# Kernel optimization log

Hardware: AMD Instinct MI355X
Metric: run time of the kernel (lower is better)

Reference implementation:

```python
import jax, jax.numpy as jnp
import numpy as np

POLY = jnp.array([-0.037, 0.481, -2.3, 4.917, -1.791], dtype=jnp.float32)


def adaptive_temperature_softmax(logits):
    # logits: [b, h, n, n]
    p = jax.nn.softmax(logits, axis=-1)
    entropy = jnp.sum(-p * jnp.log(p + 1e-9), axis=-1, keepdims=True)  # [b,h,n,1]
    poly = (POLY[0] * entropy**4 + POLY[1] * entropy**3
            + POLY[2] * entropy**2 + POLY[3] * entropy + POLY[4])
    beta = jnp.where(entropy > 0.5, jnp.maximum(poly, 1.0), 1.0)
    return jax.nn.softmax(logits * beta, axis=-1)


def setup_inputs() -> dict:
    key = jax.random.key(0)
    ks = jax.random.split(key, 5)
    b, n, dim = 2, 2048, 1024
    s = 0.02
    return {
        "x": jax.random.normal(ks[0], (b, n, dim), dtype=jnp.float32),
        "Wq": jax.random.normal(ks[1], (dim, dim), dtype=jnp.float32) * s,
        "Wk": jax.random.normal(ks[2], (dim, dim), dtype=jnp.float32) * s,
        "Wv": jax.random.normal(ks[3], (dim, dim), dtype=jnp.float32) * s,
        "Wo": jax.random.normal(ks[4], (dim, dim), dtype=jnp.float32) * s,
        "bo": jnp.zeros((dim,), dtype=jnp.float32),
    }


def reference(x, Wq, Wk, Wv, Wo, bo):
    b, n, dim = x.shape
    h = 16
    hd = dim // h

    def split_heads(t):  # [b,n,dim] -> [b,h,n,hd]
        return t.reshape(b, n, h, hd).transpose(0, 2, 1, 3)

    # torch Linear: y = x @ W.T
    q = split_heads(x @ Wq.T)
    k = split_heads(x @ Wk.T)
    v = split_heads(x @ Wv.T)

    sim = jnp.einsum('bhid,bhjd->bhij', q, k) / jnp.sqrt(jnp.float32(hd))
    causal = jnp.triu(jnp.ones((n, n), dtype=bool), 1)
    neg = -jnp.finfo(sim.dtype).max
    sim = jnp.where(causal, neg, sim)

    attn = adaptive_temperature_softmax(sim)
    out = jnp.einsum('bhij,bhjd->bhid', attn, v)
    out = out.transpose(0, 2, 1, 3).reshape(b, n, dim)
    return out @ Wo.T + bo
```

## Files before the change

kernel.cpp:

```cpp
#include <hip/hip_runtime.h>
#include <hip/hip_bf16.h>

typedef __attribute__((ext_vector_type(8))) short bf16x8;
typedef __attribute__((ext_vector_type(4))) short short4v;
typedef __attribute__((ext_vector_type(4))) float f32x4;
typedef unsigned int u32;

__device__ __forceinline__ short f2bf(float f) {
    union { float f; u32 i; } c; c.f = f;
    u32 r = c.i + 0x7FFFu + ((c.i >> 16) & 1u);
    return (short)(r >> 16);
}
__device__ __forceinline__ u32 pack2bf(float lo, float hi) {
    return ((u32)(unsigned short)f2bf(hi) << 16) | (u32)(unsigned short)f2bf(lo);
}
__device__ __forceinline__ f32x4 mfma16(bf16x8 a, bf16x8 b, f32x4 c) {
    return __builtin_amdgcn_mfma_f32_16x16x32_bf16(a, b, c, 0, 0, 0);
}
__device__ __forceinline__ f32x4 mfma16k16(short4v a, short4v b, f32x4 c) {
#if __has_builtin(__builtin_amdgcn_mfma_f32_16x16x16bf16_1k)
    return __builtin_amdgcn_mfma_f32_16x16x16bf16_1k(a, b, c, 0, 0, 0);
#else
    f32x4 d = c;
    asm volatile("v_mfma_f32_16x16x16_bf16 %0, %1, %2, %0"
                 : "+v"(d) : "v"(a), "v"(b));
    return d;
#endif
}
__device__ __forceinline__ void load_lds16(const void* g, void* l) {
    __builtin_amdgcn_global_load_lds(
        (const __attribute__((address_space(1))) u32*)g,
        (__attribute__((address_space(3))) u32*)l, 16, 0, 0);
}

__global__ __launch_bounds__(256) void cvt_all_kernel(
    const float* __restrict__ x, const float* __restrict__ wq,
    const float* __restrict__ wk, const float* __restrict__ wv,
    const float* __restrict__ wo, short* __restrict__ ws) {
    const int XV = (4096 * 1024) / 4;
    const int WV = (1024 * 1024) / 4;
    int i = blockIdx.x * 256 + threadIdx.x;
    const float4* src; short4v* dst; int off;
    if (i < XV)            { src = (const float4*)x;  dst = (short4v*)(ws);           off = i; }
    else if (i < XV + WV)  { src = (const float4*)wq; dst = (short4v*)(ws + 4194304); off = i - XV; }
    else if (i < XV + 2*WV){ src = (const float4*)wk; dst = (short4v*)(ws + 5242880); off = i - XV - WV; }
    else if (i < XV + 3*WV){ src = (const float4*)wv; dst = (short4v*)(ws + 6291456); off = i - XV - 2*WV; }
    else                   { src = (const float4*)wo; dst = (short4v*)(ws + 7340032); off = i - XV - 3*WV; }
    float4 v = src[off];
    short4v o;
    o.x = f2bf(v.x); o.y = f2bf(v.y); o.z = f2bf(v.z); o.w = f2bf(v.w);
    dst[off] = o;
}

__device__ __forceinline__ void gemm_mainloop(
    const short* __restrict__ A, const short* __restrict__ Bm,
    short* lds, int mbase, int nbase, int wave, int lane, f32x4 acc[4][4]) {
    const int K = 1024;
    const int lr = lane & 15, lg = lane >> 4;
    const int wm = wave >> 1, wn = wave & 1;
    for (int k0 = 0; k0 < K; k0 += 64) {
        __syncthreads();
        #pragma unroll
        for (int issue = 0; issue < 4; ++issue) {
            int f = issue * 4 + wave;
            int mt = f >> 1, kc = f & 1;
            load_lds16(A  + (size_t)(mbase + mt*16 + lr)*K + (k0 + kc*32 + lg*8), lds + f*512);
            load_lds16(Bm + (size_t)(nbase + mt*16 + lr)*K + (k0 + kc*32 + lg*8), lds + 8192 + f*512);
        }
        __syncthreads();
        #pragma unroll
        for (int kc = 0; kc < 2; ++kc) {
            bf16x8 af[4], bfv[4];
            #pragma unroll
            for (int mi = 0; mi < 4; ++mi)
                af[mi] = *(const bf16x8*)(lds + ((wm*4 + mi)*2 + kc)*512 + lane*8);
            #pragma unroll
            for (int ni = 0; ni < 4; ++ni)
                bfv[ni] = *(const bf16x8*)(lds + 8192 + ((wn*4 + ni)*2 + kc)*512 + lane*8);
            #pragma unroll
            for (int mi = 0; mi < 4; ++mi)
                #pragma unroll
                for (int ni = 0; ni < 4; ++ni)
                    acc[mi][ni] = mfma16(af[mi], bfv[ni], acc[mi][ni]);
        }
    }
}

__global__ __launch_bounds__(256) void gemm_qkv_kernel(
    const short* __restrict__ xb, const short* __restrict__ wqb,
    const short* __restrict__ wkb, const short* __restrict__ wvb,
    short* __restrict__ Qh, short* __restrict__ Kh, short* __restrict__ Vf) {
    __shared__ short lds[16896];
    const int wave = threadIdx.x >> 6, lane = threadIdx.x & 63;
    const int lr = lane & 15, lg = lane >> 4;
    const int sel = blockIdx.x >> 3;
    const int nbase = (blockIdx.x & 7) * 128;
    const int mbase = blockIdx.y * 128;
    const short* Bm = (sel == 0) ? wqb : (sel == 1) ? wkb : wvb;

    f32x4 acc[4][4];
    #pragma unroll
    for (int i = 0; i < 4; ++i)
        #pragma unroll
        for (int j = 0; j < 4; ++j) acc[i][j] = f32x4{0.f, 0.f, 0.f, 0.f};

    gemm_mainloop(xb, Bm, lds, mbase, nbase, wave, lane, acc);

    const int wm = wave >> 1, wn = wave & 1;
    if (sel == 2) {
        #pragma unroll
        for (int mi = 0; mi < 4; ++mi) {
            int m0 = mbase + wm*64 + mi*16 + lg*4;
            #pragma unroll
            for (int ni = 0; ni < 4; ++ni) {
                int nc = nbase + wn*64 + ni*16 + lr;
                int h = nc >> 6, d = nc & 63;
                f32x4 v = acc[mi][ni];
                int bi = m0 >> 11, np = m0 & 2047;
                int c = np >> 6, s = (np >> 4) & 3, lg2 = (np >> 2) & 3;
                int dc = d >> 4, lr2 = d & 15;
                size_t off = ((size_t)(bi*16 + h)*32 + c)*4096
                           + (size_t)((s*4 + dc)*64 + lg2*16 + lr2)*4;
                short4v o;
                o.x = f2bf(v.x); o.y = f2bf(v.y); o.z = f2bf(v.z); o.w = f2bf(v.w);
                *(short4v*)&Vf[off] = o;
            }
        }
    } else {
        short* dstb = (sel == 0) ? Qh : Kh;
        const float sc = (sel == 0) ? 0.125f : 1.0f;
        __syncthreads();
        #pragma unroll
        for (int mi = 0; mi < 4; ++mi) {
            int row0 = wm*64 + mi*16 + lg*4;
            #pragma unroll
            for (int ni = 0; ni < 4; ++ni) {
                int col = wn*64 + ni*16 + lr;
                f32x4 v = acc[mi][ni];
                #pragma unroll
                for (int r = 0; r < 4; ++r)
                    lds[(row0 + r)*132 + col] = f2bf(v[r] * sc);
            }
        }
        __syncthreads();
        const int h0 = nbase >> 6;
        const int tid = threadIdx.x;
        #pragma unroll
        for (int it = 0; it < 8; ++it) {
            int L = it*256 + tid;
            int np_l = L >> 4;
            int t16 = L & 15;
            int P = t16 >> 3;
            int c8 = (t16 & 7) * 8;
            bf16x8 val = *(const bf16x8*)&lds[np_l*132 + P*64 + c8];
            int m = mbase + np_l; int bi = m >> 11, np = m & 2047;
            *(bf16x8*)&dstb[((size_t)(bi*16 + h0 + P)*2048 + np)*64 + c8] = val;
        }
    }
}

__global__ __launch_bounds__(256) void gemm_out_kernel(
    const short* __restrict__ AO, const short* __restrict__ wob,
    const float* __restrict__ bias, float* __restrict__ out) {
    __shared__ short lds[12288];
    const int K = 1024;
    const int wave = threadIdx.x >> 6, lane = threadIdx.x & 63;
    const int lr = lane & 15, lg = lane >> 4;
    const int nbase = blockIdx.x * 128;
    const int mbase = blockIdx.y * 64;
    const int wm = wave >> 1, wn = wave & 1;

    f32x4 acc[2][4];
    #pragma unroll
    for (int i = 0; i < 2; ++i)
        #pragma unroll
        for (int j = 0; j < 4; ++j) acc[i][j] = f32x4{0.f, 0.f, 0.f, 0.f};

    for (int k0 = 0; k0 < K; k0 += 64) {
        __syncthreads();
        #pragma unroll
        for (int l = 0; l < 6; ++l) {
            int f = l*4 + wave;
            if (f < 8) {
                int mt = f >> 1, kc = f & 1;
                load_lds16(AO + (size_t)(mbase + mt*16 + lr)*K + (k0 + kc*32 + lg*8),
                           lds + f*512);
            } else {
                int fb = f - 8, nt = fb >> 1, kc = fb & 1;
                load_lds16(wob + (size_t)(nbase + nt*16 + lr)*K + (k0 + kc*32 + lg*8),
                           lds + 4096 + fb*512);
            }
        }
        __syncthreads();
        #pragma unroll
        for (int kc = 0; kc < 2; ++kc) {
            bf16x8 af[2], bfv[4];
            #pragma unroll
            for (int mi = 0; mi < 2; ++mi)
                af[mi] = *(const bf16x8*)(lds + ((wm*2 + mi)*2 + kc)*512 + lane*8);
            #pragma unroll
            for (int ni = 0; ni < 4; ++ni)
                bfv[ni] = *(const bf16x8*)(lds + 4096 + ((wn*4 + ni)*2 + kc)*512 + lane*8);
            #pragma unroll
            for (int mi = 0; mi < 2; ++mi)
                #pragma unroll
                for (int ni = 0; ni < 4; ++ni)
                    acc[mi][ni] = mfma16(af[mi], bfv[ni], acc[mi][ni]);
        }
    }

    #pragma unroll
    for (int mi = 0; mi < 2; ++mi) {
        int m0 = mbase + wm*32 + mi*16 + lg*4;
        #pragma unroll
        for (int ni = 0; ni < 4; ++ni) {
            int nc = nbase + wn*64 + ni*16 + lr;
            float bj = bias[nc];
            f32x4 v = acc[mi][ni];
            #pragma unroll
            for (int r = 0; r < 4; ++r)
                out[(size_t)(m0 + r)*1024 + nc] = v[r] + bj;
        }
    }
}

__global__ __launch_bounds__(256, 4) void attn_kernel(
    const short* __restrict__ Qh, const short* __restrict__ Kh,
    const short* __restrict__ Vf, short* __restrict__ AO) {
    __shared__ short lds[16384];
    const int lane = threadIdx.x & 63;
    const int wave = threadIdx.x >> 6;
    const int lr = lane & 15, lg = lane >> 4;
    const int bid  = blockIdx.x;
    const int xcd  = bid & 7;
    const int rest = bid >> 3;
    const int u    = 31 - (rest >> 2);
    const int bh   = ((rest & 3) << 3) | xcd;
    const int b = bh >> 4, h = bh & 15;
    const int qbase = u*64 + wave*16;
    const int qa = qbase + lr;
    const short* Q  = Qh + (size_t)bh * (2048 * 64);
    const short* Kg = Kh + (size_t)bh * (2048 * 64);
    const short* Vg = Vf + (size_t)bh * (32 * 4096);

    bf16x8 qf0 = *(const bf16x8*)&Q[(size_t)qa*64 + lg*8];
    bf16x8 qf1 = *(const bf16x8*)&Q[(size_t)qa*64 + 32 + lg*8];

    const int fc0 = wave * 2;

    auto stageK = [&](int buf, int c) {
        #pragma unroll
        for (int i = 0; i < 2; ++i) {
            int fc = fc0 + i, s = fc >> 1, ch = fc & 1;
            load_lds16(Kg + ((size_t)(c*64 + s*16 + lr)*64 + ch*32 + lg*8),
                       &lds[buf*4096 + fc*512]);
        }
    };
    auto stageV = [&](int buf, int c) {
        #pragma unroll
        for (int i = 0; i < 2; ++i) {
            int fi = fc0 + i;
            load_lds16(Vg + (size_t)c*4096 + fi*512 + lane*8,
                       &lds[8192 + buf*4096 + fi*512]);
        }
    };

    float sm = 0.f, tm = 0.f;
    stageK(0, 0);
    #pragma unroll 1
    for (int c = 0; c <= u; ++c) {
        __syncthreads();
        if (c < u) stageK((c + 1) & 1, c + 1);
        const int base = (c & 1) * 4096;
        #pragma unroll
        for (int s = 0; s < 4; ++s) {
            int k0 = c*64 + s*16;
            if (k0 <= qbase) {
                bf16x8 kf0 = *(const bf16x8*)&lds[base + (s*2    )*512 + lane*8];
                bf16x8 kf1 = *(const bf16x8*)&lds[base + (s*2 + 1)*512 + lane*8];
                f32x4 d = {0.f,0.f,0.f,0.f};
                d = mfma16(kf0, qf0, d); d = mfma16(kf1, qf1, d);
                if (k0 < qbase) {
                    #pragma unroll
                    for (int r = 0; r < 4; ++r) {
                        float e = __expf(d[r]); sm += e; tm += e * d[r];
                    }
                } else {
                    int kb = k0 + lg*4;
                    #pragma unroll
                    for (int r = 0; r < 4; ++r) {
                        float l = (kb + r <= qa) ? d[r] : -1e30f;
                        float e = __expf(l); sm += e; tm += e * l;
                    }
                }
            }
        }
    }
    sm += __shfl_xor(sm, 16); tm += __shfl_xor(tm, 16);
    sm += __shfl_xor(sm, 32); tm += __shfl_xor(tm, 32);
    float H = __logf(sm) - tm / sm;
    float beta = 1.f;
    if (H > 0.5f)
        beta = fmaxf((((-0.037f*H + 0.481f)*H - 2.3f)*H + 4.917f)*H - 1.791f, 1.f);

    f32x4 o0 = {0.f,0.f,0.f,0.f}, o1 = {0.f,0.f,0.f,0.f};
    f32x4 o2 = {0.f,0.f,0.f,0.f}, o3 = {0.f,0.f,0.f,0.f};
    float s2 = 0.f;
    __syncthreads();
    stageK(0, 0); stageV(0, 0);
    #pragma unroll 1
    for (int c = 0; c <= u; ++c) {
        __syncthreads();
        if (c < u) { stageK((c + 1) & 1, c + 1); stageV((c + 1) & 1, c + 1); }
        const int kb_ = (c & 1) * 4096;
        const int vb_ = 8192 + (c & 1) * 4096;
        #pragma unroll
        for (int s = 0; s < 4; ++s) {
            int k0 = c*64 + s*16;
            if (k0 <= qbase) {
                bf16x8 kf0 = *(const bf16x8*)&lds[kb_ + (s*2    )*512 + lane*8];
                bf16x8 kf1 = *(const bf16x8*)&lds[kb_ + (s*2 + 1)*512 + lane*8];
                f32x4 d = {0.f,0.f,0.f,0.f};
                d = mfma16(kf0, qf0, d); d = mfma16(kf1, qf1, d);
                float pv[4];
                if (k0 < qbase) {
                    #pragma unroll
                    for (int r = 0; r < 4; ++r) { pv[r] = __expf(beta * d[r]); s2 += pv[r]; }
                } else {
                    int kb = k0 + lg*4;
                    #pragma unroll
                    for (int r = 0; r < 4; ++r) {
                        pv[r] = (kb + r <= qa) ? __expf(beta * d[r]) : 0.f; s2 += pv[r];
                    }
                }
                union { short4v s4; u32 uu[2]; } pb;
                pb.uu[0] = pack2bf(pv[0], pv[1]);
                pb.uu[1] = pack2bf(pv[2], pv[3]);
                short4v vf0 = *(const short4v*)&lds[vb_ + ((s*4 + 0)*64 + lane)*4];
                short4v vf1 = *(const short4v*)&lds[vb_ + ((s*4 + 1)*64 + lane)*4];
                short4v vf2 = *(const short4v*)&lds[vb_ + ((s*4 + 2)*64 + lane)*4];
                short4v vf3 = *(const short4v*)&lds[vb_ + ((s*4 + 3)*64 + lane)*4];
                o0 = mfma16k16(vf0, pb.s4, o0);
                o1 = mfma16k16(vf1, pb.s4, o1);
                o2 = mfma16k16(vf2, pb.s4, o2);
                o3 = mfma16k16(vf3, pb.s4, o3);
            }
        }
    }
    s2 += __shfl_xor(s2, 16); s2 += __shfl_xor(s2, 32);
    float inv = 1.f / s2;

    size_t row = ((size_t)(b*2048 + qa))*1024 + h*64;
    f32x4 oo[4] = {o0, o1, o2, o3};
    #pragma unroll
    for (int dc = 0; dc < 4; ++dc) {
        short4v wv;
        #pragma unroll
        for (int r = 0; r < 4; ++r) wv[r] = f2bf(oo[dc][r] * inv);
        *(short4v*)&AO[row + dc*16 + lg*4] = wv;
    }
}

extern "C" void kernel_launch(void* const* d_in, const int* in_sizes, int n_in,
                              void* d_out, int out_size, void* d_ws, size_t ws_size,
                              hipStream_t stream) {
    const float* x  = (const float*)d_in[0];
    const float* Wq = (const float*)d_in[1];
    const float* Wk = (const float*)d_in[2];
    const float* Wv = (const float*)d_in[3];
    const float* Wo = (const float*)d_in[4];
    const float* bo = (const float*)d_in[5];
    float* out = (float*)d_out;
    short* ws = (short*)d_ws;

    short* xb  = ws;
    short* wqb = ws + 4194304;
    short* wkb = ws + 5242880;
    short* wvb = ws + 6291456;
    short* wob = ws + 7340032;
    short* Qh  = ws + 8388608;
    short* Kh  = ws + 12582912;
    short* Vf  = ws + 16777216;
    short* AO  = ws + 20971520;

    cvt_all_kernel<<<8192, 256, 0, stream>>>(x, Wq, Wk, Wv, Wo, ws);
    gemm_qkv_kernel<<<dim3(24, 32), 256, 0, stream>>>(xb, wqb, wkb, wvb, Qh, Kh, Vf);
    attn_kernel<<<1024, 256, 0, stream>>>(Qh, Kh, Vf, AO);
    gemm_out_kernel<<<dim3(8, 64), 256, 0, stream>>>(AO, wob, bo, out);
}
```

Before: 158.2 us.

## Fold log2e into Q scale for exp2 softmax and halve QKV GEMM M-tile

Q is pre-scaled by log2(e) in the QKV GEMM epilogue so the attention kernel can use raw v_exp_f32 (exp2) in place of __expf, and the entropy is recomputed in base 2 then converted back with ln2. The QKV projection GEMM tile drops from 128x128 to 64x128, doubling the grid to 1536 blocks to raise occupancy and CU coverage on the 4096x1024x3072 problem. The exp change removes a multiply per exponential in the two softmax passes. The smaller tile lowers data reuse per block and adds more global loads.

```diff
diff --git a/kernel.cpp b/kernel.cpp
--- a/kernel.cpp
+++ b/kernel.cpp
@@ -25,6 +25,13 @@
     asm volatile("v_mfma_f32_16x16x16_bf16 %0, %1, %2, %0"
                  : "+v"(d) : "v"(a), "v"(b));
     return d;
+#endif
+}
+__device__ __forceinline__ float fexp2(float x) {
+#if __has_builtin(__builtin_amdgcn_exp2f)
+    return __builtin_amdgcn_exp2f(x);
+#else
+    float r; asm("v_exp_f32 %0, %1" : "=v"(r) : "v"(x)); return r;
 #endif
 }
 __device__ __forceinline__ void load_lds16(const void* g, void* l) {
@@ -52,65 +59,63 @@
     dst[off] = o;
 }
 
-__device__ __forceinline__ void gemm_mainloop(
-    const short* __restrict__ A, const short* __restrict__ Bm,
-    short* lds, int mbase, int nbase, int wave, int lane, f32x4 acc[4][4]) {
-    const int K = 1024;
-    const int lr = lane & 15, lg = lane >> 4;
-    const int wm = wave >> 1, wn = wave & 1;
-    for (int k0 = 0; k0 < K; k0 += 64) {
-        __syncthreads();
-        #pragma unroll
-        for (int issue = 0; issue < 4; ++issue) {
-            int f = issue * 4 + wave;
-            int mt = f >> 1, kc = f & 1;
-            load_lds16(A  + (size_t)(mbase + mt*16 + lr)*K + (k0 + kc*32 + lg*8), lds + f*512);
-            load_lds16(Bm + (size_t)(nbase + mt*16 + lr)*K + (k0 + kc*32 + lg*8), lds + 8192 + f*512);
-        }
-        __syncthreads();
-        #pragma unroll
-        for (int kc = 0; kc < 2; ++kc) {
-            bf16x8 af[4], bfv[4];
-            #pragma unroll
-            for (int mi = 0; mi < 4; ++mi)
-                af[mi] = *(const bf16x8*)(lds + ((wm*4 + mi)*2 + kc)*512 + lane*8);
-            #pragma unroll
-            for (int ni = 0; ni < 4; ++ni)
-                bfv[ni] = *(const bf16x8*)(lds + 8192 + ((wn*4 + ni)*2 + kc)*512 + lane*8);
-            #pragma unroll
-            for (int mi = 0; mi < 4; ++mi)
-                #pragma unroll
-                for (int ni = 0; ni < 4; ++ni)
-                    acc[mi][ni] = mfma16(af[mi], bfv[ni], acc[mi][ni]);
-        }
-    }
-}
-
 __global__ __launch_bounds__(256) void gemm_qkv_kernel(
     const short* __restrict__ xb, const short* __restrict__ wqb,
     const short* __restrict__ wkb, const short* __restrict__ wvb,
     short* __restrict__ Qh, short* __restrict__ Kh, short* __restrict__ Vf) {
-    __shared__ short lds[16896];
+    __shared__ short lds[12288];
+    const int K = 1024;
     const int wave = threadIdx.x >> 6, lane = threadIdx.x & 63;
     const int lr = lane & 15, lg = lane >> 4;
     const int sel = blockIdx.x >> 3;
     const int nbase = (blockIdx.x & 7) * 128;
-    const int mbase = blockIdx.y * 128;
+    const int mbase = blockIdx.y * 64;
     const short* Bm = (sel == 0) ? wqb : (sel == 1) ? wkb : wvb;
-
-    f32x4 acc[4][4];
+    const int wm = wave >> 1, wn = wave & 1;
+
+    f32x4 acc[2][4];
     #pragma unroll
-    for (int i = 0; i < 4; ++i)
+    for (int i = 0; i < 2; ++i)
         #pragma unroll
         for (int j = 0; j < 4; ++j) acc[i][j] = f32x4{0.f, 0.f, 0.f, 0.f};
 
-    gemm_mainloop(xb, Bm, lds, mbase, nbase, wave, lane, acc);
-
-    const int wm = wave >> 1, wn = wave & 1;
+    for (int k0 = 0; k0 < K; k0 += 64) {
+        __syncthreads();
+        #pragma unroll
+        for (int l = 0; l < 6; ++l) {
+            int f = l*4 + wave;
+            if (f < 8) {
+                int mt = f >> 1, kc = f & 1;
+                load_lds16(xb + (size_t)(mbase + mt*16 + lr)*K + (k0 + kc*32 + lg*8),
+                           lds + f*512);
+            } else {
+                int fb = f - 8, nt = fb >> 1, kc = fb & 1;
+                load_lds16(Bm + (size_t)(nbase + nt*16 + lr)*K + (k0 + kc*32 + lg*8),
+                           lds + 4096 + fb*512);
+            }
+        }
+        __syncthreads();
+        #pragma unroll
+        for (int kc = 0; kc < 2; ++kc) {
+            bf16x8 af[2], bfv[4];
+            #pragma unroll
+            for (int mi = 0; mi < 2; ++mi)
+                af[mi] = *(const bf16x8*)(lds + ((wm*2 + mi)*2 + kc)*512 + lane*8);
+            #pragma unroll
+            for (int ni = 0; ni < 4; ++ni)
+                bfv[ni] = *(const bf16x8*)(lds + 4096 + ((wn*4 + ni)*2 + kc)*512 + lane*8);
+            #pragma unroll
+            for (int mi = 0; mi < 2; ++mi)
+                #pragma unroll
+                for (int ni = 0; ni < 4; ++ni)
+                    acc[mi][ni] = mfma16(af[mi], bfv[ni], acc[mi][ni]);
+        }
+    }
+
     if (sel == 2) {
         #pragma unroll
-        for (int mi = 0; mi < 4; ++mi) {
-            int m0 = mbase + wm*64 + mi*16 + lg*4;
+        for (int mi = 0; mi < 2; ++mi) {
+            int m0 = mbase + wm*32 + mi*16 + lg*4;
             #pragma unroll
             for (int ni = 0; ni < 4; ++ni) {
                 int nc = nbase + wn*64 + ni*16 + lr;
@@ -128,11 +133,11 @@
         }
     } else {
         short* dstb = (sel == 0) ? Qh : Kh;
-        const float sc = (sel == 0) ? 0.125f : 1.0f;
-        __syncthreads();
-        #pragma unroll
-        for (int mi = 0; mi < 4; ++mi) {
-            int row0 = wm*64 + mi*16 + lg*4;
+        const float sc = (sel == 0) ? 0.125f * 1.44269504f : 1.0f;
+        __syncthreads();
+        #pragma unroll
+        for (int mi = 0; mi < 2; ++mi) {
+            int row0 = wm*32 + mi*16 + lg*4;
             #pragma unroll
             for (int ni = 0; ni < 4; ++ni) {
                 int col = wn*64 + ni*16 + lr;
@@ -146,10 +151,10 @@
         const int h0 = nbase >> 6;
         const int tid = threadIdx.x;
         #pragma unroll
-        for (int it = 0; it < 8; ++it) {
-            int L = it*256 + tid;
-            int np_l = L >> 4;
-            int t16 = L & 15;
+        for (int it = 0; it < 4; ++it) {
+            int g = it*256 + tid;
+            int np_l = g >> 4;
+            int t16 = g & 15;
             int P = t16 >> 3;
             int c8 = (t16 & 7) * 8;
             bf16x8 val = *(const bf16x8*)&lds[np_l*132 + P*64 + c8];
@@ -265,7 +270,7 @@
         }
     };
 
-    float sm = 0.f, tm = 0.f;
+    float sm = 0.f, t2m = 0.f;
     stageK(0, 0);
     #pragma unroll 1
     for (int c = 0; c <= u; ++c) {
@@ -283,22 +288,23 @@
                 if (k0 < qbase) {
                     #pragma unroll
                     for (int r = 0; r < 4; ++r) {
-                        float e = __expf(d[r]); sm += e; tm += e * d[r];
+                        float e = fexp2(d[r]); sm += e; t2m += e * d[r];
                     }
                 } else {
                     int kb = k0 + lg*4;
                     #pragma unroll
                     for (int r = 0; r < 4; ++r) {
-                        float l = (kb + r <= qa) ? d[r] : -1e30f;
-                        float e = __expf(l); sm += e; tm += e * l;
+                        float dd = (kb + r <= qa) ? d[r] : -1e30f;
+                        float e = fexp2(dd); sm += e; t2m += e * dd;
                     }
                 }
             }
         }
     }
-    sm += __shfl_xor(sm, 16); tm += __shfl_xor(tm, 16);
-    sm += __shfl_xor(sm, 32); tm += __shfl_xor(tm, 32);
-    float H = __logf(sm) - tm / sm;
+    sm += __shfl_xor(sm, 16); t2m += __shfl_xor(t2m, 16);
+    sm += __shfl_xor(sm, 32); t2m += __shfl_xor(t2m, 32);
+    const float LN2 = 0.69314718f;
+    float H = LN2 * (__log2f(sm) - t2m / sm);
     float beta = 1.f;
     if (H > 0.5f)
         beta = fmaxf((((-0.037f*H + 0.481f)*H - 2.3f)*H + 4.917f)*H - 1.791f, 1.f);
@@ -325,12 +331,13 @@
                 float pv[4];
                 if (k0 < qbase) {
                     #pragma unroll
-                    for (int r = 0; r < 4; ++r) { pv[r] = __expf(beta * d[r]); s2 += pv[r]; }
+                    for (int r = 0; r < 4; ++r) { pv[r] = fexp2(beta * d[r]); s2 += pv[r]; }
                 } else {
                     int kb = k0 + lg*4;
                     #pragma unroll
                     for (int r = 0; r < 4; ++r) {
-                        pv[r] = (kb + r <= qa) ? __expf(beta * d[r]) : 0.f; s2 += pv[r];
+                        float dd = (kb + r <= qa) ? d[r] : -1e30f;
+                        pv[r] = fexp2(beta * dd); s2 += pv[r];
                     }
                 }
                 union { short4v s4; u32 uu[2]; } pb;
@@ -384,7 +391,7 @@
     short* AO  = ws + 20971520;
 
     cvt_all_kernel<<<8192, 256, 0, stream>>>(x, Wq, Wk, Wv, Wo, ws);
-    gemm_qkv_kernel<<<dim3(24, 32), 256, 0, stream>>>(xb, wqb, wkb, wvb, Qh, Kh, Vf);
+    gemm_qkv_kernel<<<dim3(24, 64), 256, 0, stream>>>(xb, wqb, wkb, wvb, Qh, Kh, Vf);
     attn_kernel<<<1024, 256, 0, stream>>>(Qh, Kh, Vf, AO);
     gemm_out_kernel<<<dim3(8, 64), 256, 0, stream>>>(AO, wob, bo, out);
 }
```

After: 164.3 us. 1.04x slower.
